# Optimization experiments

Measured on AMD Instinct MI355X. Metric: run time of the kernel, lower is better.

The kernel has to match this reference:

```python
import jax, jax.numpy as jnp
import numpy as np
import math

B, S, E, H = 4, 2048, 1024, 16
D = E // H  # head_dim = 64


def setup_inputs() -> dict:
    key = jax.random.key(0)
    ks = jax.random.split(key, 12)
    sc = 1.0 / math.sqrt(E)
    inp = {
        "x": jax.random.normal(ks[0], (B, S, E), jnp.float32),
        "mask": jnp.ones((B, S), jnp.int32),
        "text_array": jax.random.normal(ks[1], (B, E), jnp.float32),
        # attention projections, torch Linear convention W:[out,in]
        "Wq": jax.random.normal(ks[2], (E, E), jnp.float32) * sc,
        "bq": jnp.zeros((E,), jnp.float32),
        "Wk": jax.random.normal(ks[3], (E, E), jnp.float32) * sc,
        "bk": jnp.zeros((E,), jnp.float32),
        "Wv": jax.random.normal(ks[4], (E, E), jnp.float32) * sc,
        "bv": jnp.zeros((E,), jnp.float32),
        "Wo": jax.random.normal(ks[5], (E, E), jnp.float32) * sc,
        "bo": jnp.zeros((E,), jnp.float32),
        # TwoLayerMLP head: E -> E//2 -> 1
        "W1": jax.random.normal(ks[6], (E // 2, E), jnp.float32) * sc,
        "b1": jnp.zeros((E // 2,), jnp.float32),
        "W2": jax.random.normal(ks[7], (1, E // 2), jnp.float32) * (1.0 / math.sqrt(E // 2)),
        "b2": jnp.zeros((1,), jnp.float32),
    }
    return inp


def reference(x, mask, text_array, Wq, bq, Wk, bk, Wv, bv, Wo, bo, W1, b1, W2, b2):
    b, s, e = x.shape
    # projections -> [B, S, H, D]
    Q = (x @ Wq.T + bq).reshape(b, s, H, D)
    K = (x @ Wk.T + bk).reshape(b, s, H, D)
    V = (x @ Wv.T + bv).reshape(b, s, H, D)
    # scores [B, H, Sq, Sk]
    scores = jnp.einsum("bqhd,bkhd->bhqk", Q, K) / jnp.sqrt(jnp.asarray(D, x.dtype))
    neg_inf = jnp.asarray(-jnp.inf, scores.dtype)
    scores = jnp.where(mask[:, None, None, :] == 0, neg_inf, scores)
    attn = jax.nn.softmax(scores, axis=-1)  # dropout is identity in eval
    out = jnp.einsum("bhqk,bkhd->bqhd", attn, V).reshape(b, s, e)
    out = out @ Wo.T + bo  # out_proj (out_dropout identity)
    out = out.mean(axis=1)  # [B, E]
    out = out / jnp.linalg.norm(out, axis=-1, keepdims=True)
    out = out - text_array
    h = jax.nn.relu(out @ W1.T + b1)
    score = jnp.tanh(h @ W2.T + b2)  # [B, 1]
    return score
```

## Files before the change

kernel.cpp:

```cpp
#include <hip/hip_runtime.h>

typedef unsigned short ushort_t;
typedef unsigned int uint32;
typedef __attribute__((ext_vector_type(8))) short short8;
typedef __attribute__((ext_vector_type(4))) float f32x4;

__device__ __forceinline__ ushort_t f2bf(float f) {
  uint32 u = __builtin_bit_cast(uint32, f);
  u = (u + 0x7fffu + ((u >> 16) & 1u)) >> 16;
  return (ushort_t)u;
}

__device__ __forceinline__ float fast_exp2(float x) {
#if __has_builtin(__builtin_amdgcn_exp2f)
  return __builtin_amdgcn_exp2f(x);
#else
  return exp2f(x);
#endif
}

__device__ __forceinline__ void gload_lds16(const void* g, void* l) {
  __builtin_amdgcn_global_load_lds(
      (const __attribute__((address_space(1))) void*)g,
      (__attribute__((address_space(3))) void*)l, 16, 0, 0);
}

#define MFMA16(a, b, c) __builtin_amdgcn_mfma_f32_16x16x32_bf16((a), (b), (c), 0, 0, 0)

__global__ void cvt_all(const float* __restrict__ x, const float* __restrict__ Wq,
                        const float* __restrict__ Wk, const float* __restrict__ Wv,
                        ushort_t* __restrict__ xb, ushort_t* __restrict__ wqk,
                        ushort_t* __restrict__ wv) {
  int i = blockIdx.x * 256 + threadIdx.x;
  const float* src;
  ushort_t* dst;
  int off;
  if (i < 1048576) {
    src = x; dst = xb; off = i;
  } else if (i < 1048576 + 131072) {
    src = Wq; dst = wqk; off = i - 1048576;
  } else if (i < 1048576 + 262144) {
    src = Wk; dst = wqk + 1048576; off = i - (1048576 + 131072);
  } else {
    src = Wv; dst = wv; off = i - (1048576 + 262144);
  }
  const f32x4* s4 = (const f32x4*)src;
  f32x4 a = s4[2 * off], b = s4[2 * off + 1];
  short8 o;
  o[0] = (short)f2bf(a.x); o[1] = (short)f2bf(a.y); o[2] = (short)f2bf(a.z); o[3] = (short)f2bf(a.w);
  o[4] = (short)f2bf(b.x); o[5] = (short)f2bf(b.y); o[6] = (short)f2bf(b.z); o[7] = (short)f2bf(b.w);
  *(short8*)(dst + 8 * off) = o;
}

__global__ void maskbias_kernel(const int* __restrict__ mask, float* __restrict__ bias, int n) {
  int i = blockIdx.x * 256 + threadIdx.x;
  if (i < n) bias[i] = mask[i] ? 0.f : -30000.f;
}

__global__ __launch_bounds__(256, 2) void gemm_qk(const ushort_t* __restrict__ A,
                                                  const ushort_t* __restrict__ Bt,
                                                  const float* __restrict__ bq,
                                                  const float* __restrict__ bk,
                                                  ushort_t* __restrict__ Qb,
                                                  ushort_t* __restrict__ Kb, float qscale) {
  __shared__ ushort_t As[2][128 * 32];
  __shared__ ushort_t Bs[2][128 * 32];
  const int K = 1024;
  const int tid = threadIdx.x;
  const int w = tid >> 6, l = tid & 63;
  const int wr = w >> 1, wc = w & 1;
  const int lr = l & 15, g = l >> 4;
  const int bm = blockIdx.y * 128, bn = blockIdx.x * 128;
  const bool isq = bn < 1024;

  const char* gA = (const char*)(A + (size_t)(bm + w * 32 + (l >> 2)) * K + (l & 3) * 8);
  const char* gB = (const char*)(Bt + (size_t)(bn + w * 32 + (l >> 2)) * K + (l & 3) * 8);
  const size_t rowstep = (size_t)16 * K * 2;

  f32x4 acc[4][4] = {};

  auto stage = [&](int buf, int k0) {
    char* dA = (char*)&As[buf][0] + w * 2048;
    char* dB = (char*)&Bs[buf][0] + w * 2048;
    const char* sA = gA + (size_t)k0 * 2;
    const char* sB = gB + (size_t)k0 * 2;
    gload_lds16(sA, dA);
    gload_lds16(sA + rowstep, dA + 1024);
    gload_lds16(sB, dB);
    gload_lds16(sB + rowstep, dB + 1024);
  };

  stage(0, 0);
  __syncthreads();

  const int nk = K >> 5;
  for (int kk = 0; kk < nk; kk++) {
    const int cur = kk & 1;
    if (kk + 1 < nk) stage(cur ^ 1, (kk + 1) << 5);
    short8 af[4], bf[4];
#pragma unroll
    for (int fm = 0; fm < 4; fm++)
      af[fm] = *(const short8*)(&As[cur][(wr * 64 + fm * 16 + lr) * 32 + g * 8]);
#pragma unroll
    for (int fn = 0; fn < 4; fn++)
      bf[fn] = *(const short8*)(&Bs[cur][(wc * 64 + fn * 16 + lr) * 32 + g * 8]);
#pragma unroll
    for (int fm = 0; fm < 4; fm++)
#pragma unroll
      for (int fn = 0; fn < 4; fn++) acc[fm][fn] = MFMA16(af[fm], bf[fn], acc[fm][fn]);
    __syncthreads();
  }

  const float* bias = isq ? bq : bk;
  ushort_t* C = isq ? Qb : Kb;
  const float scale = isq ? qscale : 1.0f;
#pragma unroll
  for (int fn = 0; fn < 4; fn++) {
    int col = bn + wc * 64 + fn * 16 + lr;
    int colh = col & 1023;
    float bv = bias[colh];
    int h = colh >> 6, d = colh & 63;
#pragma unroll
    for (int fm = 0; fm < 4; fm++) {
      int rowb = bm + wr * 64 + fm * 16 + g * 4;
#pragma unroll
      for (int j = 0; j < 4; j++) {
        int row = rowb + j;
        int b = row >> 11, s = row & 2047;
        float v = (acc[fm][fn][j] + bv) * scale;
        C[((size_t)(b * 16 + h) * 2048 + s) * 64 + d] = f2bf(v);
      }
    }
  }
}

__global__ __launch_bounds__(256, 2) void gemm_vf(const ushort_t* __restrict__ A,
                                                  const ushort_t* __restrict__ Bt,
                                                  const float* __restrict__ bias,
                                                  float* __restrict__ C) {
  __shared__ ushort_t As[2][128 * 32];
  __shared__ ushort_t Bs[2][128 * 32];
  const int K = 1024;
  const int tid = threadIdx.x;
  const int w = tid >> 6, l = tid & 63;
  const int wr = w >> 1, wc = w & 1;
  const int lr = l & 15, g = l >> 4;
  const int bm = blockIdx.y * 128, bn = blockIdx.x * 128;

  const char* gA = (const char*)(A + (size_t)(bm + w * 32 + (l >> 2)) * K + (l & 3) * 8);
  const char* gB = (const char*)(Bt + (size_t)(bn + w * 32 + (l >> 2)) * K + (l & 3) * 8);
  const size_t rowstep = (size_t)16 * K * 2;

  f32x4 acc[4][4] = {};

  auto stage = [&](int buf, int k0) {
    char* dA = (char*)&As[buf][0] + w * 2048;
    char* dB = (char*)&Bs[buf][0] + w * 2048;
    const char* sA = gA + (size_t)k0 * 2;
    const char* sB = gB + (size_t)k0 * 2;
    gload_lds16(sA, dA);
    gload_lds16(sA + rowstep, dA + 1024);
    gload_lds16(sB, dB);
    gload_lds16(sB + rowstep, dB + 1024);
  };

  stage(0, 0);
  __syncthreads();

  const int nk = K >> 5;
  for (int kk = 0; kk < nk; kk++) {
    const int cur = kk & 1;
    if (kk + 1 < nk) stage(cur ^ 1, (kk + 1) << 5);
    short8 af[4], bf[4];
#pragma unroll
    for (int fm = 0; fm < 4; fm++)
      af[fm] = *(const short8*)(&As[cur][(wr * 64 + fm * 16 + lr) * 32 + g * 8]);
#pragma unroll
    for (int fn = 0; fn < 4; fn++)
      bf[fn] = *(const short8*)(&Bs[cur][(wc * 64 + fn * 16 + lr) * 32 + g * 8]);
#pragma unroll
    for (int fm = 0; fm < 4; fm++)
#pragma unroll
      for (int fn = 0; fn < 4; fn++) acc[fm][fn] = MFMA16(af[fm], bf[fn], acc[fm][fn]);
    __syncthreads();
  }

#pragma unroll
  for (int fn = 0; fn < 4; fn++) {
    int col = bn + wc * 64 + fn * 16 + lr;
    float bv = bias[col];
#pragma unroll
    for (int fm = 0; fm < 4; fm++) {
      int rowb = bm + wr * 64 + fm * 16 + g * 4;
#pragma unroll
      for (int j = 0; j < 4; j++) {
        C[(size_t)(rowb + j) * 1024 + col] = acc[fm][fn][j] + bv;
      }
    }
  }
}

__global__ __launch_bounds__(256, 3) void qk_stats(const ushort_t* __restrict__ Qb,
                                                   const ushort_t* __restrict__ Kb,
                                                   const float* __restrict__ mbias,
                                                   float* __restrict__ cq) {
  __shared__ ushort_t Ks[2][64 * 64];
  const int tid = threadIdx.x;
  const int w = tid >> 6, l = tid & 63;
  const int g = l >> 4, qi = l & 15;
  const int xr = qi & 7;
  const int qblk = blockIdx.x, bh = blockIdx.y;
  const int b = bh >> 4;
  const int q0 = qblk * 128 + w * 32;

  short8 qf[2][2];
#pragma unroll
  for (int qh = 0; qh < 2; qh++) {
    const ushort_t* qp = Qb + ((size_t)bh * 2048 + q0 + qh * 16 + qi) * 64 + g * 8;
    qf[qh][0] = *(const short8*)qp;
    qf[qh][1] = *(const short8*)(qp + 32);
  }

  const int srow = l >> 3;
  const int sch = (l & 7) ^ srow;
  const char* gK = (const char*)Kb + ((size_t)bh * 2048 + w * 8 + srow) * 128 + sch * 16;
  const float* bbase = mbias + b * 2048 + g * 4;

  auto stage = [&](int buf, int t) {
    const char* sK = gK + (size_t)t * (64 * 128);
    char* dK = (char*)&Ks[buf][0] + w * 1024;
    gload_lds16(sK, dK);
    gload_lds16(sK + 32 * 128, dK + 4096);
  };

  float mrun[2] = {-1e30f, -1e30f}, lsum[2] = {0.f, 0.f};
  stage(0, 0);
  __syncthreads();

  for (int t = 0; t < 32; t++) {
    const int cur = t & 1;
    f32x4 bvec[4];
#pragma unroll
    for (int fn = 0; fn < 4; fn++) bvec[fn] = *(const f32x4*)(bbase + t * 64 + fn * 16);

    if (t < 31) stage(cur ^ 1, t + 1);

    short8 kf[4][2];
#pragma unroll
    for (int fn = 0; fn < 4; fn++) {
      const ushort_t* kr = &Ks[cur][(fn * 16 + qi) * 64];
      kf[fn][0] = *(const short8*)(kr + (g ^ xr) * 8);
      kf[fn][1] = *(const short8*)(kr + ((4 + g) ^ xr) * 8);
    }

#pragma unroll
    for (int qh = 0; qh < 2; qh++) {
      f32x4 sc[4];
#pragma unroll
      for (int fn = 0; fn < 4; fn++) {
        f32x4 z = {};
        z = MFMA16(kf[fn][0], qf[qh][0], z);
        z = MFMA16(kf[fn][1], qf[qh][1], z);
        sc[fn] = z;
      }
      float pmax = -1e30f;
#pragma unroll
      for (int fn = 0; fn < 4; fn++)
#pragma unroll
        for (int j = 0; j < 4; j++) {
          float v = sc[fn][j] + bvec[fn][j];
          sc[fn][j] = v;
          pmax = fmaxf(pmax, v);
        }
      pmax = fmaxf(pmax, __shfl_xor(pmax, 16));
      pmax = fmaxf(pmax, __shfl_xor(pmax, 32));
      if (__any(pmax > mrun[qh] + 8.f)) {
        float mnew = fmaxf(mrun[qh], pmax);
        lsum[qh] *= fast_exp2(mrun[qh] - mnew);
        mrun[qh] = mnew;
      }
      const float m = mrun[qh];
      float psum = 0.f;
#pragma unroll
      for (int fn = 0; fn < 4; fn++) {
        float p0 = fast_exp2(sc[fn][0] - m);
        float p1 = fast_exp2(sc[fn][1] - m);
        float p2 = fast_exp2(sc[fn][2] - m);
        float p3 = fast_exp2(sc[fn][3] - m);
        psum += (p0 + p1) + (p2 + p3);
      }
      psum += __shfl_xor(psum, 16);
      psum += __shfl_xor(psum, 32);
      lsum[qh] += psum;
    }
    __syncthreads();
  }

#pragma unroll
  for (int qh = 0; qh < 2; qh++)
    if (l < 16) cq[(size_t)bh * 2048 + q0 + qh * 16 + l] = mrun[qh] + __log2f(lsum[qh]);
}

__global__ __launch_bounds__(256, 2) void wsum_v(const ushort_t* __restrict__ Qb,
                                                 const ushort_t* __restrict__ Kb,
                                                 const float* __restrict__ Vf,
                                                 const float* __restrict__ mbias,
                                                 const float* __restrict__ cq,
                                                 float* __restrict__ meanO) {
  __shared__ ushort_t Qs[2][64 * 64];
  __shared__ float wl[4][64];
  const int tid = threadIdx.x;
  const int w = tid >> 6, l = tid & 63;
  const int g = l >> 4, qi = l & 15;
  const int xr = qi & 7;
  const int kvb = blockIdx.x, bh = blockIdx.y;
  const int b = bh >> 4, h = bh & 15;
  const int kv0 = kvb * 256 + w * 64;

  short8 kf[4][2];
#pragma unroll
  for (int fn = 0; fn < 4; fn++) {
    const ushort_t* kp = Kb + ((size_t)bh * 2048 + kv0 + fn * 16 + qi) * 64 + g * 8;
    kf[fn][0] = *(const short8*)kp;
    kf[fn][1] = *(const short8*)(kp + 32);
  }
  f32x4 bvec[4];
#pragma unroll
  for (int fn = 0; fn < 4; fn++)
    bvec[fn] = *(const f32x4*)(mbias + b * 2048 + kv0 + fn * 16 + g * 4);

  const int srow = l >> 3, sch = (l & 7) ^ srow;
  const char* gQ = (const char*)Qb + ((size_t)bh * 2048 + w * 8 + srow) * 128 + sch * 16;
  auto stageQ = [&](int buf, int t) {
    const char* sQ = gQ + (size_t)t * (64 * 128);
    char* dQ = (char*)&Qs[buf][0] + w * 1024;
    gload_lds16(sQ, dQ);
    gload_lds16(sQ + 32 * 128, dQ + 4096);
  };

  f32x4 acc[4] = {};
  const float* cqb = cq + (size_t)bh * 2048;
  stageQ(0, 0);
  __syncthreads();

  for (int t = 0; t < 32; t++) {
    const int cur = t & 1;
    if (t < 31) stageQ(cur ^ 1, t + 1);
#pragma unroll
    for (int sub = 0; sub < 4; sub++) {
      const ushort_t* qr = &Qs[cur][(sub * 16 + qi) * 64];
      short8 q0f = *(const short8*)(qr + (g ^ xr) * 8);
      short8 q1f = *(const short8*)(qr + ((4 + g) ^ xr) * 8);
      float cv = cqb[t * 64 + sub * 16 + qi];
#pragma unroll
      for (int fn = 0; fn < 4; fn++) {
        f32x4 z = {};
        z = MFMA16(kf[fn][0], q0f, z);
        z = MFMA16(kf[fn][1], q1f, z);
#pragma unroll
        for (int j = 0; j < 4; j++) acc[fn][j] += fast_exp2(z[j] + bvec[fn][j] - cv);
      }
    }
    __syncthreads();
  }

#pragma unroll
  for (int msk = 1; msk < 16; msk <<= 1) {
#pragma unroll
    for (int fn = 0; fn < 4; fn++) {
      acc[fn][0] += __shfl_xor(acc[fn][0], msk);
      acc[fn][1] += __shfl_xor(acc[fn][1], msk);
      acc[fn][2] += __shfl_xor(acc[fn][2], msk);
      acc[fn][3] += __shfl_xor(acc[fn][3], msk);
    }
  }
  if (qi == 0) {
#pragma unroll
    for (int fn = 0; fn < 4; fn++)
#pragma unroll
      for (int j = 0; j < 4; j++) wl[w][fn * 16 + g * 4 + j] = acc[fn][j];
  }
  __syncthreads();

  float od = 0.f;
  const float* vrow = Vf + (size_t)(b * 2048 + kv0) * 1024 + h * 64 + l;
  const float* wp = wl[w];
#pragma unroll 8
  for (int k = 0; k < 64; k++) od += wp[k] * vrow[(size_t)k * 1024];
  atomicAdd(&meanO[b * 1024 + h * 64 + l], od);
}

__global__ void proj_o(const float* __restrict__ meanO, const float* __restrict__ Wo,
                       const float* __restrict__ bo, float* __restrict__ y) {
  int b = blockIdx.y;
  int t = threadIdx.x;
  int n = blockIdx.x * 64 + (t >> 2);
  int part = t & 3;
  const f32x4* wrow = (const f32x4*)(Wo + (size_t)n * 1024 + part * 256);
  const f32x4* mo = (const f32x4*)(meanO + b * 1024 + part * 256);
  float acc = 0.f;
#pragma unroll 8
  for (int i = 0; i < 64; i++) {
    f32x4 wv = wrow[i], mv = mo[i];
    acc += wv.x * mv.x + wv.y * mv.y + wv.z * mv.z + wv.w * mv.w;
  }
  acc += __shfl_xor(acc, 1);
  acc += __shfl_xor(acc, 2);
  if (part == 0) y[b * 1024 + n] = acc * (1.0f / 2048.0f) + bo[n];
}

__global__ void tail_kernel(const float* __restrict__ y, const float* __restrict__ text,
                            const float* __restrict__ W1, const float* __restrict__ b1,
                            const float* __restrict__ W2, const float* __restrict__ b2,
                            float* __restrict__ out) {
  __shared__ float u[1024];
  __shared__ float hbuf[512];
  __shared__ float red[8];
  int b = blockIdx.x, t = threadIdx.x;
  const float* yb = y + b * 1024;

  float ss = 0.f;
  for (int i = t; i < 1024; i += 256) {
    float v = yb[i];
    ss += v * v;
  }
  for (int m = 1; m < 64; m <<= 1) ss += __shfl_xor(ss, m);
  if ((t & 63) == 0) red[t >> 6] = ss;
  __syncthreads();
  float rn = rsqrtf(red[0] + red[1] + red[2] + red[3]);
  for (int i = t; i < 1024; i += 256) u[i] = yb[i] * rn - text[b * 1024 + i];
  __syncthreads();

  int grp = t >> 2, part = t & 3;
  for (int p = 0; p < 8; p++) {
    int j = p * 64 + grp;
    const f32x4* wr = (const f32x4*)(W1 + (size_t)j * 1024 + part * 256);
    const f32x4* uu = (const f32x4*)(u + part * 256);
    float a = 0.f;
#pragma unroll 8
    for (int i = 0; i < 64; i++) {
      f32x4 wv = wr[i], uv = uu[i];
      a += wv.x * uv.x + wv.y * uv.y + wv.z * uv.z + wv.w * uv.w;
    }
    a += __shfl_xor(a, 1);
    a += __shfl_xor(a, 2);
    if (part == 0) hbuf[j] = fmaxf(a + b1[j], 0.f);
  }
  __syncthreads();

  float s2 = 0.f;
  for (int j = t; j < 512; j += 256) s2 += hbuf[j] * W2[j];
  for (int m = 1; m < 64; m <<= 1) s2 += __shfl_xor(s2, m);
  if ((t & 63) == 0) red[t >> 6] = s2;
  __syncthreads();
  if (t == 0) out[b] = tanhf(red[0] + red[1] + red[2] + red[3] + b2[0]);
}

extern "C" void kernel_launch(void* const* d_in, const int* in_sizes, int n_in, void* d_out,
                              int out_size, void* d_ws, size_t ws_size, hipStream_t stream) {
  (void)in_sizes; (void)n_in; (void)out_size; (void)ws_size;
  const float* x = (const float*)d_in[0];
  const int* mask = (const int*)d_in[1];
  const float* text = (const float*)d_in[2];
  const float* Wq = (const float*)d_in[3];
  const float* bq = (const float*)d_in[4];
  const float* Wk = (const float*)d_in[5];
  const float* bk = (const float*)d_in[6];
  const float* Wv = (const float*)d_in[7];
  const float* bv = (const float*)d_in[8];
  const float* Wo = (const float*)d_in[9];
  const float* bo = (const float*)d_in[10];
  const float* W1 = (const float*)d_in[11];
  const float* b1 = (const float*)d_in[12];
  const float* W2 = (const float*)d_in[13];
  const float* b2 = (const float*)d_in[14];

  char* ws = (char*)d_ws;
  const size_t MB = 1024 * 1024;
  ushort_t* Qb = (ushort_t*)(ws);
  ushort_t* Kb = (ushort_t*)(ws + 16 * MB);
  float* Vf = (float*)(ws + 32 * MB);
  ushort_t* xb = (ushort_t*)(ws + 64 * MB);
  ushort_t* wqk = (ushort_t*)(ws + 80 * MB);
  ushort_t* wvb = (ushort_t*)(ws + 84 * MB);
  float* cq = (float*)(ws + 86 * MB);
  float* meanO = (float*)(ws + 87 * MB);
  float* y = (float*)(ws + 87 * MB + 16384);
  float* mbias = (float*)(ws + 87 * MB + 65536);

  cvt_all<<<5632, 256, 0, stream>>>(x, Wq, Wk, Wv, xb, wqk, wvb);
  maskbias_kernel<<<32, 256, 0, stream>>>(mask, mbias, 8192);
  hipMemsetAsync(meanO, 0, 4096 * sizeof(float), stream);

  const float qscale = 0.125f * 1.44269504088896f;
  gemm_qk<<<dim3(16, 64), 256, 0, stream>>>(xb, wqk, bq, bk, Qb, Kb, qscale);
  gemm_vf<<<dim3(8, 64), 256, 0, stream>>>(xb, wvb, bv, Vf);

  qk_stats<<<dim3(16, 64), 256, 0, stream>>>(Qb, Kb, mbias, cq);
  wsum_v<<<dim3(8, 64), 256, 0, stream>>>(Qb, Kb, Vf, mbias, cq, meanO);

  proj_o<<<dim3(16, 4), 256, 0, stream>>>(meanO, Wo, bo, y);
  tail_kernel<<<4, 256, 0, stream>>>(y, text, W1, b1, W2, b2, (float*)d_out);
}
```

Before: 401.9 us.

## Fold mask bias into convert kernel, split MLP tail, raise attention occupancy bounds

Folds the mask-to-bias conversion into the bf16 convert kernel, which removes one launch. Splits the single 4-block tail kernel into norm, a parallel 32-block MLP layer-1 kernel, and an MLP layer-2 kernel, so the W1 GEMV is spread over more CUs. Raises the launch_bounds occupancy hints on qk_stats and wsum_v, which may force the compiler to use fewer registers and risks spills. The tail now takes two extra launches, but each launch is short.

Result: faster. 358.7 us (-10.7%).

```diff
diff --git a/kernel.cpp b/kernel.cpp
--- a/kernel.cpp
+++ b/kernel.cpp
@@ -4,6 +4,7 @@
 typedef unsigned int uint32;
 typedef __attribute__((ext_vector_type(8))) short short8;
 typedef __attribute__((ext_vector_type(4))) float f32x4;
+typedef __attribute__((ext_vector_type(4))) int int4v;
 
 __device__ __forceinline__ ushort_t f2bf(float f) {
   uint32 u = __builtin_bit_cast(uint32, f);
@@ -29,9 +30,25 @@
 
 __global__ void cvt_all(const float* __restrict__ x, const float* __restrict__ Wq,
                         const float* __restrict__ Wk, const float* __restrict__ Wv,
-                        ushort_t* __restrict__ xb, ushort_t* __restrict__ wqk,
-                        ushort_t* __restrict__ wv) {
+                        const int* __restrict__ mask, ushort_t* __restrict__ xb,
+                        ushort_t* __restrict__ wqk, ushort_t* __restrict__ wv,
+                        float* __restrict__ mbias) {
   int i = blockIdx.x * 256 + threadIdx.x;
+  if (i >= 1441792) {
+    int off = (i - 1441792) * 8;
+    if (off < 8192) {
+      int4v m0 = *(const int4v*)(mask + off);
+      int4v m1 = *(const int4v*)(mask + off + 4);
+      f32x4 b0, b1;
+      b0.x = m0.x ? 0.f : -30000.f; b0.y = m0.y ? 0.f : -30000.f;
+      b0.z = m0.z ? 0.f : -30000.f; b0.w = m0.w ? 0.f : -30000.f;
+      b1.x = m1.x ? 0.f : -30000.f; b1.y = m1.y ? 0.f : -30000.f;
+      b1.z = m1.z ? 0.f : -30000.f; b1.w = m1.w ? 0.f : -30000.f;
+      *(f32x4*)(mbias + off) = b0;
+      *(f32x4*)(mbias + off + 4) = b1;
+    }
+    return;
+  }
   const float* src;
   ushort_t* dst;
   int off;
@@ -50,11 +67,6 @@
   o[0] = (short)f2bf(a.x); o[1] = (short)f2bf(a.y); o[2] = (short)f2bf(a.z); o[3] = (short)f2bf(a.w);
   o[4] = (short)f2bf(b.x); o[5] = (short)f2bf(b.y); o[6] = (short)f2bf(b.z); o[7] = (short)f2bf(b.w);
   *(short8*)(dst + 8 * off) = o;
-}
-
-__global__ void maskbias_kernel(const int* __restrict__ mask, float* __restrict__ bias, int n) {
-  int i = blockIdx.x * 256 + threadIdx.x;
-  if (i < n) bias[i] = mask[i] ? 0.f : -30000.f;
 }
 
 __global__ __launch_bounds__(256, 2) void gemm_qk(const ushort_t* __restrict__ A,
@@ -200,7 +212,7 @@
   }
 }
 
-__global__ __launch_bounds__(256, 3) void qk_stats(const ushort_t* __restrict__ Qb,
+__global__ __launch_bounds__(256, 4) void qk_stats(const ushort_t* __restrict__ Qb,
                                                    const ushort_t* __restrict__ Kb,
                                                    const float* __restrict__ mbias,
                                                    float* __restrict__ cq) {
@@ -301,7 +313,7 @@
     if (l < 16) cq[(size_t)bh * 2048 + q0 + qh * 16 + l] = mrun[qh] + __log2f(lsum[qh]);
 }
 
-__global__ __launch_bounds__(256, 2) void wsum_v(const ushort_t* __restrict__ Qb,
+__global__ __launch_bounds__(256, 3) void wsum_v(const ushort_t* __restrict__ Qb,
                                                  const ushort_t* __restrict__ Kb,
                                                  const float* __restrict__ Vf,
                                                  const float* __restrict__ mbias,
@@ -409,16 +421,11 @@
   if (part == 0) y[b * 1024 + n] = acc * (1.0f / 2048.0f) + bo[n];
 }
 
-__global__ void tail_kernel(const float* __restrict__ y, const float* __restrict__ text,
-                            const float* __restrict__ W1, const float* __restrict__ b1,
-                            const float* __restrict__ W2, const float* __restrict__ b2,
-                            float* __restrict__ out) {
-  __shared__ float u[1024];
-  __shared__ float hbuf[512];
-  __shared__ float red[8];
+__global__ void norm_kernel(const float* __restrict__ y, const float* __restrict__ text,
+                            float* __restrict__ u) {
+  __shared__ float red[4];
   int b = blockIdx.x, t = threadIdx.x;
   const float* yb = y + b * 1024;
-
   float ss = 0.f;
   for (int i = t; i < 1024; i += 256) {
     float v = yb[i];
@@ -428,28 +435,34 @@
   if ((t & 63) == 0) red[t >> 6] = ss;
   __syncthreads();
   float rn = rsqrtf(red[0] + red[1] + red[2] + red[3]);
-  for (int i = t; i < 1024; i += 256) u[i] = yb[i] * rn - text[b * 1024 + i];
-  __syncthreads();
-
-  int grp = t >> 2, part = t & 3;
-  for (int p = 0; p < 8; p++) {
-    int j = p * 64 + grp;
-    const f32x4* wr = (const f32x4*)(W1 + (size_t)j * 1024 + part * 256);
-    const f32x4* uu = (const f32x4*)(u + part * 256);
-    float a = 0.f;
+  for (int i = t; i < 1024; i += 256) u[b * 1024 + i] = yb[i] * rn - text[b * 1024 + i];
+}
+
+__global__ void mlp1_kernel(const float* __restrict__ u, const float* __restrict__ W1,
+                            const float* __restrict__ b1, float* __restrict__ hb) {
+  int b = blockIdx.y;
+  int t = threadIdx.x;
+  int j = blockIdx.x * 64 + (t >> 2);
+  int part = t & 3;
+  const f32x4* wr = (const f32x4*)(W1 + (size_t)j * 1024 + part * 256);
+  const f32x4* uu = (const f32x4*)(u + b * 1024 + part * 256);
+  float a = 0.f;
 #pragma unroll 8
-    for (int i = 0; i < 64; i++) {
-      f32x4 wv = wr[i], uv = uu[i];
-      a += wv.x * uv.x + wv.y * uv.y + wv.z * uv.z + wv.w * uv.w;
-    }
-    a += __shfl_xor(a, 1);
-    a += __shfl_xor(a, 2);
-    if (part == 0) hbuf[j] = fmaxf(a + b1[j], 0.f);
-  }
-  __syncthreads();
-
+  for (int i = 0; i < 64; i++) {
+    f32x4 wv = wr[i], uv = uu[i];
+    a += wv.x * uv.x + wv.y * uv.y + wv.z * uv.z + wv.w * uv.w;
+  }
+  a += __shfl_xor(a, 1);
+  a += __shfl_xor(a, 2);
+  if (part == 0) hb[b * 512 + j] = fmaxf(a + b1[j], 0.f);
+}
+
+__global__ void mlp2_kernel(const float* __restrict__ hb, const float* __restrict__ W2,
+                            const float* __restrict__ b2, float* __restrict__ out) {
+  __shared__ float red[4];
+  int b = blockIdx.x, t = threadIdx.x;
   float s2 = 0.f;
-  for (int j = t; j < 512; j += 256) s2 += hbuf[j] * W2[j];
+  for (int j = t; j < 512; j += 256) s2 += hb[b * 512 + j] * W2[j];
   for (int m = 1; m < 64; m <<= 1) s2 += __shfl_xor(s2, m);
   if ((t & 63) == 0) red[t >> 6] = s2;
   __syncthreads();
@@ -486,10 +499,11 @@
   float* cq = (float*)(ws + 86 * MB);
   float* meanO = (float*)(ws + 87 * MB);
   float* y = (float*)(ws + 87 * MB + 16384);
+  float* u = (float*)(ws + 87 * MB + 32768);
+  float* hb = (float*)(ws + 87 * MB + 49152);
   float* mbias = (float*)(ws + 87 * MB + 65536);
 
-  cvt_all<<<5632, 256, 0, stream>>>(x, Wq, Wk, Wv, xb, wqk, wvb);
-  maskbias_kernel<<<32, 256, 0, stream>>>(mask, mbias, 8192);
+  cvt_all<<<5636, 256, 0, stream>>>(x, Wq, Wk, Wv, mask, xb, wqk, wvb, mbias);
   hipMemsetAsync(meanO, 0, 4096 * sizeof(float), stream);
 
   const float qscale = 0.125f * 1.44269504088896f;
@@ -500,5 +514,7 @@
   wsum_v<<<dim3(8, 64), 256, 0, stream>>>(Qb, Kb, Vf, mbias, cq, meanO);
 
   proj_o<<<dim3(16, 4), 256, 0, stream>>>(meanO, Wo, bo, y);
-  tail_kernel<<<4, 256, 0, stream>>>(y, text, W1, b1, W2, b2, (float*)d_out);
-}
+  norm_kernel<<<4, 256, 0, stream>>>(y, text, u);
+  mlp1_kernel<<<dim3(8, 4), 256, 0, stream>>>(u, W1, b1, hb);
+  mlp2_kernel<<<4, 256, 0, stream>>>(hb, W2, b2, (float*)d_out);
+}
```
